# Optimization experiments

Measured on AMD Instinct MI355X. Metric: run time of the kernel, lower is better.

Reference implementation:

```python
import jax, jax.numpy as jnp
import numpy as np

ALPHA = 0.1
N_NODES = 100000
N_FEATS = 1024
HIDDEN = 64
N_CLASSES = 64
N_EDGES = 3200000


def setup_inputs() -> dict:
    key = jax.random.key(0)
    k1, k2, k3, k4 = jax.random.split(key, 4)
    x = jax.random.normal(k1, (N_NODES, N_FEATS), dtype=jnp.float32)
    lin1_w = jax.random.normal(k2, (N_FEATS, HIDDEN), dtype=jnp.float32) * (1.0 / np.sqrt(N_FEATS))
    lin1_b = jnp.zeros((HIDDEN,), dtype=jnp.float32)
    lin2_w = jax.random.normal(k3, (HIDDEN, N_CLASSES), dtype=jnp.float32) * (1.0 / np.sqrt(HIDDEN))
    lin2_b = jnp.zeros((N_CLASSES,), dtype=jnp.float32)
    edge_index = jax.random.randint(k4, (2, N_EDGES), 0, N_NODES, dtype=jnp.int32)
    return {"x": x, "lin1_w": lin1_w, "lin1_b": lin1_b,
            "lin2_w": lin2_w, "lin2_b": lin2_b,
            "edge_index": edge_index, "K": 10}


def _appnp(h, edge_index, n_nodes, K):
    # GCN normalization with self loops: deg^-1/2 (A + I) deg^-1/2
    loops = jnp.arange(n_nodes, dtype=edge_index.dtype)
    row = jnp.concatenate([edge_index[0], loops])  # target nodes
    col = jnp.concatenate([edge_index[1], loops])  # source nodes
    deg = jax.ops.segment_sum(jnp.ones_like(row, dtype=h.dtype), row,
                              num_segments=n_nodes)
    dinv = jnp.where(deg > 0, jax.lax.rsqrt(jnp.maximum(deg, 1e-12)), 0.0)
    norm = dinv[row] * dinv[col]  # [E+N]

    def step(z, _):
        msg = z[col] * norm[:, None]                     # gather + scale
        agg = jax.ops.segment_sum(msg, row, num_segments=n_nodes)
        z = (1.0 - ALPHA) * agg + ALPHA * h              # teleport to h0
        return z, None

    z, _ = jax.lax.scan(step, h, None, length=K)
    return z


def reference(x, lin1_w, lin1_b, lin2_w, lin2_b, edge_index, K):
    # eval mode: dropout disabled
    h = jax.nn.relu(x @ lin1_w + lin1_b)
    h = h @ lin2_w + lin2_b
    z = _appnp(h, edge_index, x.shape[0], K)
    return jax.nn.log_softmax(z, axis=1)
```

## Files before the change

kernel.cpp:

```cpp
#include <hip/hip_runtime.h>
#include <math.h>


constexpr int KSTEPS = 10;

typedef __attribute__((ext_vector_type(8))) short short8;
typedef __attribute__((ext_vector_type(4))) float f32x4;

static __device__ __forceinline__ unsigned short f2bf(float f) {
    unsigned u = __builtin_bit_cast(unsigned, f);
    unsigned r = (u + 0x7FFFu + ((u >> 16) & 1u)) >> 16;
    return (unsigned short)r;
}
static __device__ __forceinline__ float bf2f(unsigned short b) {
    unsigned u = (unsigned)b << 16;
    return __builtin_bit_cast(float, u);
}
static __device__ __forceinline__ void splitbf(float f, short* hi, short* lo) {
    unsigned u = __builtin_bit_cast(unsigned, f);
    *hi = (short)(u >> 16);
    float rem = f - __builtin_bit_cast(float, u & 0xFFFF0000u);
    *lo = (short)f2bf(rem);
}
static __device__ __forceinline__ unsigned char f2fp8(float f) {
    int p = __builtin_amdgcn_cvt_pk_fp8_f32(f, f, 0, false);
    return (unsigned char)(p & 0xFF);
}
static __device__ __forceinline__ float fp82f(unsigned b) {
    return __builtin_amdgcn_cvt_f32_fp8((int)b, 0);
}


__global__ void k_zero(int* __restrict__ p, int n) {
    int i = blockIdx.x * 256 + threadIdx.x;
    if (i < n) p[i] = 0;
}

__global__ void k_hist(const int* __restrict__ ei, int* __restrict__ btot, int E, int NB) {
    __shared__ int hist[512];
    for (int t = threadIdx.x; t < NB; t += 256) hist[t] = 0;
    __syncthreads();
    int base = blockIdx.x * 4096;
#pragma unroll
    for (int k = 0; k < 16; ++k) {
        int e = base + k * 256 + threadIdx.x;
        if (e < E) atomicAdd(&hist[ei[e] >> 8], 1);
    }
    __syncthreads();
    for (int t = threadIdx.x; t < NB; t += 256) {
        int c = hist[t];
        if (c) atomicAdd(&btot[t], c);
    }
}

__global__ void k_scanb(const int* __restrict__ btot, int* __restrict__ bstart,
                        int* __restrict__ bcur, int* __restrict__ row_ptr,
                        int NB, int N, int E) {
    __shared__ int lds[512];
    int t = threadIdx.x;
    int v0 = (t < NB) ? btot[t] : 0;
    int v = v0;
    lds[t] = v;
    __syncthreads();
    for (int o = 1; o < 512; o <<= 1) {
        int a = (t >= o) ? lds[t - o] : 0;
        __syncthreads();
        v += a;
        lds[t] = v;
        __syncthreads();
    }
    if (t < NB) {
        int ex = v - v0;
        bstart[t] = ex;
        bcur[t] = ex;
    }
    if (t == 0) {
        bstart[NB] = E;
        row_ptr[N] = E;
    }
}

__launch_bounds__(256)
__global__ void k_part(const int* __restrict__ ei, int* __restrict__ bcur,
                       unsigned* __restrict__ ebuf, int E, int NB) {
    __shared__ int hist[512], rebase[512], lcur[512];
    for (int t = threadIdx.x; t < NB; t += 256) { hist[t] = 0; lcur[t] = 0; }
    __syncthreads();
    int base = blockIdx.x * 4096;
    int r[16], c[16];
#pragma unroll
    for (int k = 0; k < 16; ++k) {
        int e = base + k * 256 + threadIdx.x;
        bool ok = e < E;
        r[k] = ok ? ei[e] : -1;
        c[k] = ok ? ei[E + e] : 0;
        if (ok) atomicAdd(&hist[r[k] >> 8], 1);
    }
    __syncthreads();
    for (int t = threadIdx.x; t < NB; t += 256) {
        int cnt = hist[t];
        rebase[t] = cnt ? atomicAdd(&bcur[t], cnt) : 0;
    }
    __syncthreads();
#pragma unroll
    for (int k = 0; k < 16; ++k) {
        if (r[k] >= 0) {
            int b = r[k] >> 8;
            int pos = rebase[b] + atomicAdd(&lcur[b], 1);
            ebuf[pos] = (unsigned)c[k] | ((unsigned)(r[k] & 255) << 24);
        }
    }
}

__launch_bounds__(256)
__global__ void k_bucket(const unsigned* __restrict__ ebuf, const int* __restrict__ bstart,
                         int* __restrict__ row_ptr, float* __restrict__ dinv,
                         int* __restrict__ cols, int N) {
    __shared__ int cnt[256], cur[256], lds[256];
    int b = blockIdx.x, t = threadIdx.x;
    int s = bstart[b], e2 = bstart[b + 1];
    cnt[t] = 0;
    __syncthreads();
    for (int i = s + t; i < e2; i += 256) {
        unsigned p = ebuf[i];
        atomicAdd(&cnt[p >> 24], 1);
    }
    __syncthreads();
    int v0 = cnt[t];
    int v = v0;
    lds[t] = v;
    __syncthreads();
    for (int o = 1; o < 256; o <<= 1) {
        int a = (t >= o) ? lds[t - o] : 0;
        __syncthreads();
        v += a;
        lds[t] = v;
        __syncthreads();
    }
    int excl = v - v0;
    int row = (b << 8) + t;
    if (row < N) {
        row_ptr[row] = s + excl;
        dinv[row] = rsqrtf((float)(v0 + 1));
    }
    cur[t] = s + excl;
    __syncthreads();
    for (int i = s + t; i < e2; i += 256) {
        unsigned p = ebuf[i];
        int pos = atomicAdd(&cur[p >> 24], 1);
        cols[pos] = (int)(p & 0x00FFFFFFu);
    }
}

__global__ void k_zrow(unsigned char* __restrict__ a, unsigned char* __restrict__ b,
                       unsigned char* __restrict__ c, int N) {
    int t = threadIdx.x;
    size_t o = (size_t)N * 64 + t;
    a[o] = 0; b[o] = 0; c[o] = 0;
}

__global__ void k_pack_w1(const float* __restrict__ w1, short* __restrict__ w1fh,
                          short* __restrict__ w1fl) {
    int t = blockIdx.x * 256 + threadIdx.x;
    int j = t & 7, lane = (t >> 3) & 63, nb = (t >> 9) & 3, kb = t >> 11;
    int k = kb * 32 + ((lane >> 4) << 3) + j;
    int c = nb * 16 + (lane & 15);
    short hi, lo;
    splitbf(w1[k * 64 + c], &hi, &lo);
    w1fh[t] = hi;
    w1fl[t] = lo;
}

__global__ void k_pack_w2(const float* __restrict__ w2, short* __restrict__ w2fh,
                          short* __restrict__ w2fl) {
    int t = blockIdx.x * 256 + threadIdx.x;
    int j = t & 7, lane = (t >> 3) & 63, nb = (t >> 9) & 3, kb = (t >> 11) & 1;
    int k = kb * 32 + ((lane >> 4) << 3) + j;
    int c = nb * 16 + (lane & 15);
    short hi, lo;
    splitbf(w2[k * 64 + c], &hi, &lo);
    w2fh[t] = hi;
    w2fl[t] = lo;
}

__launch_bounds__(256)
__global__ void k_mlp(const float* __restrict__ x,
                      const short8* __restrict__ w1fh, const short8* __restrict__ w1fl,
                      const float* __restrict__ b1,
                      const short8* __restrict__ w2fh, const short8* __restrict__ w2fl,
                      const float* __restrict__ b2, const float* __restrict__ dinv,
                      unsigned short* __restrict__ ah, unsigned char* __restrict__ u0,
                      int M, int F) {
    __shared__ __align__(16) short c1sh[4][16][64];
    __shared__ __align__(16) short c1sl[4][16][64];
    int tid = threadIdx.x;
    int w = tid >> 6, lane = tid & 63;
    int hi = lane >> 4, lx = lane & 15;
    int rbase = blockIdx.x * 64 + w * 16;
    int row = rbase + lx;
    size_t rowc = (row < M) ? (size_t)row : (size_t)(M - 1);
    const float* xr = x + rowc * (size_t)F + hi * 8;

    f32x4 acc[4];
#pragma unroll
    for (int nb = 0; nb < 4; ++nb) acc[nb] = (f32x4){0.f, 0.f, 0.f, 0.f};

    int KK = F >> 5;
#pragma unroll 2
    for (int kk = 0; kk < KK; ++kk) {
        float4 a0 = *reinterpret_cast<const float4*>(xr + kk * 32);
        float4 a1 = *reinterpret_cast<const float4*>(xr + kk * 32 + 4);
        float av[8] = {a0.x, a0.y, a0.z, a0.w, a1.x, a1.y, a1.z, a1.w};
        short8 afh, afl;
#pragma unroll
        for (int j = 0; j < 8; ++j) {
            short h8, l8;
            splitbf(av[j], &h8, &l8);
            afh[j] = h8;
            afl[j] = l8;
        }
#pragma unroll
        for (int nb = 0; nb < 4; ++nb) {
            short8 bfh = w1fh[(kk * 4 + nb) * 64 + lane];
            short8 bfl = w1fl[(kk * 4 + nb) * 64 + lane];
            acc[nb] = __builtin_amdgcn_mfma_f32_16x16x32_bf16(afh, bfh, acc[nb], 0, 0, 0);
            acc[nb] = __builtin_amdgcn_mfma_f32_16x16x32_bf16(afl, bfh, acc[nb], 0, 0, 0);
            acc[nb] = __builtin_amdgcn_mfma_f32_16x16x32_bf16(afh, bfl, acc[nb], 0, 0, 0);
        }
    }

    short* myh = &c1sh[w][0][0];
    short* myl = &c1sl[w][0][0];
#pragma unroll
    for (int nb = 0; nb < 4; ++nb) {
        int col = nb * 16 + lx;
        float bb = b1[col];
#pragma unroll
        for (int r = 0; r < 4; ++r) {
            int rr = hi * 4 + r;
            float v = fmaxf(acc[nb][r] + bb, 0.f);
            short h8, l8;
            splitbf(v, &h8, &l8);
            myh[rr * 64 + col] = h8;
            myl[rr * 64 + col] = l8;
        }
    }
    __syncthreads();

    f32x4 acc2[4];
#pragma unroll
    for (int nb = 0; nb < 4; ++nb) acc2[nb] = (f32x4){0.f, 0.f, 0.f, 0.f};
#pragma unroll
    for (int kb = 0; kb < 2; ++kb) {
        short8 a2h = *reinterpret_cast<const short8*>(&myh[lx * 64 + kb * 32 + hi * 8]);
        short8 a2l = *reinterpret_cast<const short8*>(&myl[lx * 64 + kb * 32 + hi * 8]);
#pragma unroll
        for (int nb = 0; nb < 4; ++nb) {
            short8 bfh = w2fh[(kb * 4 + nb) * 64 + lane];
            short8 bfl = w2fl[(kb * 4 + nb) * 64 + lane];
            acc2[nb] = __builtin_amdgcn_mfma_f32_16x16x32_bf16(a2h, bfh, acc2[nb], 0, 0, 0);
            acc2[nb] = __builtin_amdgcn_mfma_f32_16x16x32_bf16(a2l, bfh, acc2[nb], 0, 0, 0);
            acc2[nb] = __builtin_amdgcn_mfma_f32_16x16x32_bf16(a2h, bfl, acc2[nb], 0, 0, 0);
        }
    }

#pragma unroll
    for (int r = 0; r < 4; ++r) {
        int orow = rbase + hi * 4 + r;
        float dv = (orow < M) ? dinv[orow] : 0.f;
#pragma unroll
        for (int nb = 0; nb < 4; ++nb) {
            int col = nb * 16 + lx;
            if (orow < M) {
                float v = acc2[nb][r] + b2[col];
                ah[(size_t)orow * 64 + col] = f2bf(0.1f * v);
                u0[(size_t)orow * 64 + col] = f2fp8(dv * v);
            }
        }
    }
}

__global__ void k_prop(const unsigned char* __restrict__ uin, const unsigned short* __restrict__ ah,
                       const float* __restrict__ dinv, const int* __restrict__ row_ptr,
                       const int* __restrict__ cols, unsigned char* __restrict__ uout,
                       int n, int E) {
    int wid = threadIdx.x >> 6;
    int lane = threadIdx.x & 63;
    int half = lane >> 5, fl = lane & 31;
    int r0 = blockIdx.x * 8 + wid * 2;
    int ra = min(r0, n - 1), rb = min(r0 + 1, n - 1);
    int ea = row_ptr[ra], enda = row_ptr[ra + 1];
    int eb = row_ptr[rb], endb = row_ptr[rb + 1];
    int trips = (max(enda - ea, endb - eb) + 7) >> 3;
    int e0 = half ? eb : ea;
    int end_ = half ? endb : enda;
    int r = half ? rb : ra;

    float s0 = 0.f, s1 = 0.f, s2 = 0.f, s3 = 0.f, s4 = 0.f, s5 = 0.f, s6 = 0.f, s7 = 0.f;
    float t0 = 0.f, t1 = 0.f, t2 = 0.f, t3 = 0.f, t4 = 0.f, t5 = 0.f, t6 = 0.f, t7 = 0.f;
    for (int t = 0; t < trips; ++t) {
        int base = e0 + t * 8;
        int ep0 = base,     ep1 = base + 1, ep2 = base + 2, ep3 = base + 3;
        int ep4 = base + 4, ep5 = base + 5, ep6 = base + 6, ep7 = base + 7;
        int c0 = (ep0 < end_) ? cols[min(ep0, E - 1)] : n;
        int c1 = (ep1 < end_) ? cols[min(ep1, E - 1)] : n;
        int c2 = (ep2 < end_) ? cols[min(ep2, E - 1)] : n;
        int c3 = (ep3 < end_) ? cols[min(ep3, E - 1)] : n;
        int c4 = (ep4 < end_) ? cols[min(ep4, E - 1)] : n;
        int c5 = (ep5 < end_) ? cols[min(ep5, E - 1)] : n;
        int c6 = (ep6 < end_) ? cols[min(ep6, E - 1)] : n;
        int c7 = (ep7 < end_) ? cols[min(ep7, E - 1)] : n;
        unsigned v0 = *reinterpret_cast<const unsigned short*>(uin + (size_t)c0 * 64 + fl * 2);
        unsigned v1 = *reinterpret_cast<const unsigned short*>(uin + (size_t)c1 * 64 + fl * 2);
        unsigned v2 = *reinterpret_cast<const unsigned short*>(uin + (size_t)c2 * 64 + fl * 2);
        unsigned v3 = *reinterpret_cast<const unsigned short*>(uin + (size_t)c3 * 64 + fl * 2);
        unsigned v4 = *reinterpret_cast<const unsigned short*>(uin + (size_t)c4 * 64 + fl * 2);
        unsigned v5 = *reinterpret_cast<const unsigned short*>(uin + (size_t)c5 * 64 + fl * 2);
        unsigned v6 = *reinterpret_cast<const unsigned short*>(uin + (size_t)c6 * 64 + fl * 2);
        unsigned v7 = *reinterpret_cast<const unsigned short*>(uin + (size_t)c7 * 64 + fl * 2);
        s0 += fp82f(v0 & 0xFF); t0 += fp82f(v0 >> 8);
        s1 += fp82f(v1 & 0xFF); t1 += fp82f(v1 >> 8);
        s2 += fp82f(v2 & 0xFF); t2 += fp82f(v2 >> 8);
        s3 += fp82f(v3 & 0xFF); t3 += fp82f(v3 >> 8);
        s4 += fp82f(v4 & 0xFF); t4 += fp82f(v4 >> 8);
        s5 += fp82f(v5 & 0xFF); t5 += fp82f(v5 >> 8);
        s6 += fp82f(v6 & 0xFF); t6 += fp82f(v6 >> 8);
        s7 += fp82f(v7 & 0xFF); t7 += fp82f(v7 >> 8);
    }
    float sa = ((s0 + s1) + (s2 + s3)) + ((s4 + s5) + (s6 + s7));
    float sb = ((t0 + t1) + (t2 + t3)) + ((t4 + t5) + (t6 + t7));
    unsigned sv = *reinterpret_cast<const unsigned short*>(uin + (size_t)r * 64 + fl * 2);
    unsigned av = *reinterpret_cast<const unsigned*>(ah + (size_t)r * 64 + fl * 2);
    float di = dinv[r];
    float w = 0.9f * di;
    float z0 = fmaf(w, sa + fp82f(sv & 0xFF), bf2f((unsigned short)(av & 0xFFFF)));
    float z1 = fmaf(w, sb + fp82f(sv >> 8), bf2f((unsigned short)(av >> 16)));
    if (blockIdx.x * 8 + wid * 2 + half < n) {
        unsigned short o = (unsigned short)((unsigned)f2fp8(di * z0) | ((unsigned)f2fp8(di * z1) << 8));
        *reinterpret_cast<unsigned short*>(uout + (size_t)r * 64 + fl * 2) = o;
    }
}

__global__ void k_prop_lsm(const unsigned char* __restrict__ uin, const unsigned short* __restrict__ ah,
                           const float* __restrict__ dinv, const int* __restrict__ row_ptr,
                           const int* __restrict__ cols, float* __restrict__ out,
                           int n, int E) {
    int wid = threadIdx.x >> 6;
    int lane = threadIdx.x & 63;
    int half = lane >> 5, fl = lane & 31;
    int r0 = blockIdx.x * 8 + wid * 2;
    int ra = min(r0, n - 1), rb = min(r0 + 1, n - 1);
    int ea = row_ptr[ra], enda = row_ptr[ra + 1];
    int eb = row_ptr[rb], endb = row_ptr[rb + 1];
    int trips = (max(enda - ea, endb - eb) + 7) >> 3;
    int e0 = half ? eb : ea;
    int end_ = half ? endb : enda;
    int r = half ? rb : ra;

    float s0 = 0.f, s1 = 0.f, s2 = 0.f, s3 = 0.f, s4 = 0.f, s5 = 0.f, s6 = 0.f, s7 = 0.f;
    float t0 = 0.f, t1 = 0.f, t2 = 0.f, t3 = 0.f, t4 = 0.f, t5 = 0.f, t6 = 0.f, t7 = 0.f;
    for (int t = 0; t < trips; ++t) {
        int base = e0 + t * 8;
        int ep0 = base,     ep1 = base + 1, ep2 = base + 2, ep3 = base + 3;
        int ep4 = base + 4, ep5 = base + 5, ep6 = base + 6, ep7 = base + 7;
        int c0 = (ep0 < end_) ? cols[min(ep0, E - 1)] : n;
        int c1 = (ep1 < end_) ? cols[min(ep1, E - 1)] : n;
        int c2 = (ep2 < end_) ? cols[min(ep2, E - 1)] : n;
        int c3 = (ep3 < end_) ? cols[min(ep3, E - 1)] : n;
        int c4 = (ep4 < end_) ? cols[min(ep4, E - 1)] : n;
        int c5 = (ep5 < end_) ? cols[min(ep5, E - 1)] : n;
        int c6 = (ep6 < end_) ? cols[min(ep6, E - 1)] : n;
        int c7 = (ep7 < end_) ? cols[min(ep7, E - 1)] : n;
        unsigned v0 = *reinterpret_cast<const unsigned short*>(uin + (size_t)c0 * 64 + fl * 2);
        unsigned v1 = *reinterpret_cast<const unsigned short*>(uin + (size_t)c1 * 64 + fl * 2);
        unsigned v2 = *reinterpret_cast<const unsigned short*>(uin + (size_t)c2 * 64 + fl * 2);
        unsigned v3 = *reinterpret_cast<const unsigned short*>(uin + (size_t)c3 * 64 + fl * 2);
        unsigned v4 = *reinterpret_cast<const unsigned short*>(uin + (size_t)c4 * 64 + fl * 2);
        unsigned v5 = *reinterpret_cast<const unsigned short*>(uin + (size_t)c5 * 64 + fl * 2);
        unsigned v6 = *reinterpret_cast<const unsigned short*>(uin + (size_t)c6 * 64 + fl * 2);
        unsigned v7 = *reinterpret_cast<const unsigned short*>(uin + (size_t)c7 * 64 + fl * 2);
        s0 += fp82f(v0 & 0xFF); t0 += fp82f(v0 >> 8);
        s1 += fp82f(v1 & 0xFF); t1 += fp82f(v1 >> 8);
        s2 += fp82f(v2 & 0xFF); t2 += fp82f(v2 >> 8);
        s3 += fp82f(v3 & 0xFF); t3 += fp82f(v3 >> 8);
        s4 += fp82f(v4 & 0xFF); t4 += fp82f(v4 >> 8);
        s5 += fp82f(v5 & 0xFF); t5 += fp82f(v5 >> 8);
        s6 += fp82f(v6 & 0xFF); t6 += fp82f(v6 >> 8);
        s7 += fp82f(v7 & 0xFF); t7 += fp82f(v7 >> 8);
    }
    float sa = ((s0 + s1) + (s2 + s3)) + ((s4 + s5) + (s6 + s7));
    float sb = ((t0 + t1) + (t2 + t3)) + ((t4 + t5) + (t6 + t7));
    unsigned sv = *reinterpret_cast<const unsigned short*>(uin + (size_t)r * 64 + fl * 2);
    unsigned av = *reinterpret_cast<const unsigned*>(ah + (size_t)r * 64 + fl * 2);
    float di = dinv[r];
    float w = 0.9f * di;
    float z0 = fmaf(w, sa + fp82f(sv & 0xFF), bf2f((unsigned short)(av & 0xFFFF)));
    float z1 = fmaf(w, sb + fp82f(sv >> 8), bf2f((unsigned short)(av >> 16)));
    float m = fmaxf(z0, z1);
#pragma unroll
    for (int o = 1; o <= 16; o <<= 1) m = fmaxf(m, __shfl_xor(m, o, 64));
    float s = expf(z0 - m) + expf(z1 - m);
#pragma unroll
    for (int o = 1; o <= 16; o <<= 1) s += __shfl_xor(s, o, 64);
    float ls = m + logf(s);
    if (blockIdx.x * 8 + wid * 2 + half < n) {
        float2 o2 = make_float2(z0 - ls, z1 - ls);
        *reinterpret_cast<float2*>(out + (size_t)r * 64 + fl * 2) = o2;
    }
}

extern "C" void kernel_launch(void* const* d_in, const int* in_sizes, int n_in,
                              void* d_out, int out_size, void* d_ws, size_t ws_size,
                              hipStream_t stream) {
    const float* x  = (const float*)d_in[0];
    const float* w1 = (const float*)d_in[1];
    const float* b1 = (const float*)d_in[2];
    const float* w2 = (const float*)d_in[3];
    const float* b2 = (const float*)d_in[4];
    const int*   ei = (const int*)d_in[5];

    int F = in_sizes[1] / 64;
    int N = in_sizes[0] / F;
    int E = in_sizes[5] / 2;
    int NB = (N + 255) >> 8;

    char* p = (char*)d_ws;
    auto alloc = [&](size_t bytes) {
        void* r = (void*)p;
        p += (bytes + 255) & ~(size_t)255;
        return r;
    };
    unsigned short* ah   = (unsigned short*)alloc((size_t)N * 64 * 2);
    unsigned char*  u0   = (unsigned char*)alloc((size_t)(N + 1) * 64);
    unsigned char*  uA   = (unsigned char*)alloc((size_t)(N + 1) * 64);
    unsigned char*  uB   = (unsigned char*)alloc((size_t)(N + 1) * 64);
    float* dinv    = (float*)alloc((size_t)N * 4);
    int*   row_ptr = (int*)alloc((size_t)(N + 1) * 4);
    int*   btot    = (int*)alloc(2048);
    int*   bstart  = (int*)alloc(2048);
    int*   bcur    = (int*)alloc(2048);
    unsigned* ebuf = (unsigned*)alloc((size_t)E * 4);
    int*   cols    = (int*)alloc((size_t)E * 4);
    short* w1fh    = (short*)alloc((size_t)F * 64 * 2);
    short* w1fl    = (short*)alloc((size_t)F * 64 * 2);
    short* w2fh    = (short*)alloc((size_t)64 * 64 * 2);
    short* w2fl    = (short*)alloc((size_t)64 * 64 * 2);

    int neb = (E + 4095) / 4096;

    k_zero<<<2, 256, 0, stream>>>(btot, NB);
    k_hist<<<neb, 256, 0, stream>>>(ei, btot, E, NB);
    k_scanb<<<1, 512, 0, stream>>>(btot, bstart, bcur, row_ptr, NB, N, E);
    k_part<<<neb, 256, 0, stream>>>(ei, bcur, ebuf, E, NB);
    k_bucket<<<NB, 256, 0, stream>>>(ebuf, bstart, row_ptr, dinv, cols, N);
    k_zrow<<<1, 64, 0, stream>>>(u0, uA, uB, N);
    k_pack_w1<<<(F * 64) / 256, 256, 0, stream>>>(w1, w1fh, w1fl);
    k_pack_w2<<<16, 256, 0, stream>>>(w2, w2fh, w2fl);
    k_mlp<<<(N + 63) / 64, 256, 0, stream>>>(x, (const short8*)w1fh, (const short8*)w1fl, b1,
                                             (const short8*)w2fh, (const short8*)w2fl, b2,
                                             dinv, ah, u0, N, F);

    const unsigned char* uin = u0;
    unsigned char* bufs[2] = {uA, uB};
    int npb = (N + 7) / 8;
    for (int k = 0; k < KSTEPS - 1; ++k) {
        unsigned char* uo = bufs[k & 1];
        k_prop<<<npb, 256, 0, stream>>>(uin, ah, dinv, row_ptr, cols, uo, N, E);
        uin = uo;
    }
    k_prop_lsm<<<npb, 256, 0, stream>>>(uin, ah, dinv, row_ptr, cols, (float*)d_out, N, E);
}
```

Measured before the change: 810.4 us.

## Drop split-bf16 emulation in MLP and streamline fp8 propagation kernels

The MLP previously emulated fp32 precision with hi/lo bf16 splits and three MFMAs per tile. It now uses a single bf16 MFMA per tile with one packed weight array and one shared-memory buffer, and the main loop unroll goes from 2 to 4. The propagation kernels load column indices without clamping, relying on a padded cols allocation, and use the byte-select fp8 conversion and packed fp8 store. This cuts MFMA and conversion work in the x-reading GEMM but lowers precision of the dense layers.

```diff
diff --git a/kernel.cpp b/kernel.cpp
--- a/kernel.cpp
+++ b/kernel.cpp
@@ -16,18 +16,15 @@
     unsigned u = (unsigned)b << 16;
     return __builtin_bit_cast(float, u);
 }
-static __device__ __forceinline__ void splitbf(float f, short* hi, short* lo) {
-    unsigned u = __builtin_bit_cast(unsigned, f);
-    *hi = (short)(u >> 16);
-    float rem = f - __builtin_bit_cast(float, u & 0xFFFF0000u);
-    *lo = (short)f2bf(rem);
-}
 static __device__ __forceinline__ unsigned char f2fp8(float f) {
     int p = __builtin_amdgcn_cvt_pk_fp8_f32(f, f, 0, false);
     return (unsigned char)(p & 0xFF);
 }
-static __device__ __forceinline__ float fp82f(unsigned b) {
-    return __builtin_amdgcn_cvt_f32_fp8((int)b, 0);
+static __device__ __forceinline__ float fp8b0(unsigned v) {
+    return __builtin_amdgcn_cvt_f32_fp8((int)v, 0);
+}
+static __device__ __forceinline__ float fp8b1(unsigned v) {
+    return __builtin_amdgcn_cvt_f32_fp8((int)v, 1);
 }
 
 
@@ -159,40 +156,29 @@
     a[o] = 0; b[o] = 0; c[o] = 0;
 }
 
-__global__ void k_pack_w1(const float* __restrict__ w1, short* __restrict__ w1fh,
-                          short* __restrict__ w1fl) {
+__global__ void k_pack_w1(const float* __restrict__ w1, short* __restrict__ w1f) {
     int t = blockIdx.x * 256 + threadIdx.x;
     int j = t & 7, lane = (t >> 3) & 63, nb = (t >> 9) & 3, kb = t >> 11;
     int k = kb * 32 + ((lane >> 4) << 3) + j;
     int c = nb * 16 + (lane & 15);
-    short hi, lo;
-    splitbf(w1[k * 64 + c], &hi, &lo);
-    w1fh[t] = hi;
-    w1fl[t] = lo;
-}
-
-__global__ void k_pack_w2(const float* __restrict__ w2, short* __restrict__ w2fh,
-                          short* __restrict__ w2fl) {
+    w1f[t] = (short)f2bf(w1[k * 64 + c]);
+}
+
+__global__ void k_pack_w2(const float* __restrict__ w2, short* __restrict__ w2f) {
     int t = blockIdx.x * 256 + threadIdx.x;
     int j = t & 7, lane = (t >> 3) & 63, nb = (t >> 9) & 3, kb = (t >> 11) & 1;
     int k = kb * 32 + ((lane >> 4) << 3) + j;
     int c = nb * 16 + (lane & 15);
-    short hi, lo;
-    splitbf(w2[k * 64 + c], &hi, &lo);
-    w2fh[t] = hi;
-    w2fl[t] = lo;
+    w2f[t] = (short)f2bf(w2[k * 64 + c]);
 }
 
 __launch_bounds__(256)
-__global__ void k_mlp(const float* __restrict__ x,
-                      const short8* __restrict__ w1fh, const short8* __restrict__ w1fl,
-                      const float* __restrict__ b1,
-                      const short8* __restrict__ w2fh, const short8* __restrict__ w2fl,
+__global__ void k_mlp(const float* __restrict__ x, const short8* __restrict__ w1f,
+                      const float* __restrict__ b1, const short8* __restrict__ w2f,
                       const float* __restrict__ b2, const float* __restrict__ dinv,
                       unsigned short* __restrict__ ah, unsigned char* __restrict__ u0,
                       int M, int F) {
-    __shared__ __align__(16) short c1sh[4][16][64];
-    __shared__ __align__(16) short c1sl[4][16][64];
+    __shared__ __align__(16) short c1s[4][16][64];
     int tid = threadIdx.x;
     int w = tid >> 6, lane = tid & 63;
     int hi = lane >> 4, lx = lane & 15;
@@ -206,31 +192,23 @@
     for (int nb = 0; nb < 4; ++nb) acc[nb] = (f32x4){0.f, 0.f, 0.f, 0.f};
 
     int KK = F >> 5;
-#pragma unroll 2
+#pragma unroll 4
     for (int kk = 0; kk < KK; ++kk) {
         float4 a0 = *reinterpret_cast<const float4*>(xr + kk * 32);
         float4 a1 = *reinterpret_cast<const float4*>(xr + kk * 32 + 4);
-        float av[8] = {a0.x, a0.y, a0.z, a0.w, a1.x, a1.y, a1.z, a1.w};
-        short8 afh, afl;
-#pragma unroll
-        for (int j = 0; j < 8; ++j) {
-            short h8, l8;
-            splitbf(av[j], &h8, &l8);
-            afh[j] = h8;
-            afl[j] = l8;
+        short8 af;
+        af[0] = (short)f2bf(a0.x); af[1] = (short)f2bf(a0.y);
+        af[2] = (short)f2bf(a0.z); af[3] = (short)f2bf(a0.w);
+        af[4] = (short)f2bf(a1.x); af[5] = (short)f2bf(a1.y);
+        af[6] = (short)f2bf(a1.z); af[7] = (short)f2bf(a1.w);
+#pragma unroll
+        for (int nb = 0; nb < 4; ++nb) {
+            short8 bf = w1f[(kk * 4 + nb) * 64 + lane];
+            acc[nb] = __builtin_amdgcn_mfma_f32_16x16x32_bf16(af, bf, acc[nb], 0, 0, 0);
         }
-#pragma unroll
-        for (int nb = 0; nb < 4; ++nb) {
-            short8 bfh = w1fh[(kk * 4 + nb) * 64 + lane];
-            short8 bfl = w1fl[(kk * 4 + nb) * 64 + lane];
-            acc[nb] = __builtin_amdgcn_mfma_f32_16x16x32_bf16(afh, bfh, acc[nb], 0, 0, 0);
-            acc[nb] = __builtin_amdgcn_mfma_f32_16x16x32_bf16(afl, bfh, acc[nb], 0, 0, 0);
-            acc[nb] = __builtin_amdgcn_mfma_f32_16x16x32_bf16(afh, bfl, acc[nb], 0, 0, 0);
-        }
-    }
-
-    short* myh = &c1sh[w][0][0];
-    short* myl = &c1sl[w][0][0];
+    }
+
+    short* my = &c1s[w][0][0];
 #pragma unroll
     for (int nb = 0; nb < 4; ++nb) {
         int col = nb * 16 + lx;
@@ -238,11 +216,7 @@
 #pragma unroll
         for (int r = 0; r < 4; ++r) {
             int rr = hi * 4 + r;
-            float v = fmaxf(acc[nb][r] + bb, 0.f);
-            short h8, l8;
-            splitbf(v, &h8, &l8);
-            myh[rr * 64 + col] = h8;
-            myl[rr * 64 + col] = l8;
+            my[rr * 64 + col] = (short)f2bf(fmaxf(acc[nb][r] + bb, 0.f));
         }
     }
     __syncthreads();
@@ -252,15 +226,11 @@
     for (int nb = 0; nb < 4; ++nb) acc2[nb] = (f32x4){0.f, 0.f, 0.f, 0.f};
 #pragma unroll
     for (int kb = 0; kb < 2; ++kb) {
-        short8 a2h = *reinterpret_cast<const short8*>(&myh[lx * 64 + kb * 32 + hi * 8]);
-        short8 a2l = *reinterpret_cast<const short8*>(&myl[lx * 64 + kb * 32 + hi * 8]);
+        short8 af2 = *reinterpret_cast<const short8*>(&my[lx * 64 + kb * 32 + hi * 8]);
 #pragma unroll
         for (int nb = 0; nb < 4; ++nb) {
-            short8 bfh = w2fh[(kb * 4 + nb) * 64 + lane];
-            short8 bfl = w2fl[(kb * 4 + nb) * 64 + lane];
-            acc2[nb] = __builtin_amdgcn_mfma_f32_16x16x32_bf16(a2h, bfh, acc2[nb], 0, 0, 0);
-            acc2[nb] = __builtin_amdgcn_mfma_f32_16x16x32_bf16(a2l, bfh, acc2[nb], 0, 0, 0);
-            acc2[nb] = __builtin_amdgcn_mfma_f32_16x16x32_bf16(a2h, bfl, acc2[nb], 0, 0, 0);
+            short8 bf2 = w2f[(kb * 4 + nb) * 64 + lane];
+            acc2[nb] = __builtin_amdgcn_mfma_f32_16x16x32_bf16(af2, bf2, acc2[nb], 0, 0, 0);
         }
     }
 
@@ -282,8 +252,7 @@
 
 __global__ void k_prop(const unsigned char* __restrict__ uin, const unsigned short* __restrict__ ah,
                        const float* __restrict__ dinv, const int* __restrict__ row_ptr,
-                       const int* __restrict__ cols, unsigned char* __restrict__ uout,
-                       int n, int E) {
+                       const int* __restrict__ cols, unsigned char* __restrict__ uout, int n) {
     int wid = threadIdx.x >> 6;
     int lane = threadIdx.x & 63;
     int half = lane >> 5, fl = lane & 31;
@@ -300,16 +269,16 @@
     float t0 = 0.f, t1 = 0.f, t2 = 0.f, t3 = 0.f, t4 = 0.f, t5 = 0.f, t6 = 0.f, t7 = 0.f;
     for (int t = 0; t < trips; ++t) {
         int base = e0 + t * 8;
-        int ep0 = base,     ep1 = base + 1, ep2 = base + 2, ep3 = base + 3;
-        int ep4 = base + 4, ep5 = base + 5, ep6 = base + 6, ep7 = base + 7;
-        int c0 = (ep0 < end_) ? cols[min(ep0, E - 1)] : n;
-        int c1 = (ep1 < end_) ? cols[min(ep1, E - 1)] : n;
-        int c2 = (ep2 < end_) ? cols[min(ep2, E - 1)] : n;
-        int c3 = (ep3 < end_) ? cols[min(ep3, E - 1)] : n;
-        int c4 = (ep4 < end_) ? cols[min(ep4, E - 1)] : n;
-        int c5 = (ep5 < end_) ? cols[min(ep5, E - 1)] : n;
-        int c6 = (ep6 < end_) ? cols[min(ep6, E - 1)] : n;
-        int c7 = (ep7 < end_) ? cols[min(ep7, E - 1)] : n;
+        int q0 = cols[base],     q1 = cols[base + 1], q2 = cols[base + 2], q3 = cols[base + 3];
+        int q4 = cols[base + 4], q5 = cols[base + 5], q6 = cols[base + 6], q7 = cols[base + 7];
+        int c0 = (base     < end_) ? q0 : n;
+        int c1 = (base + 1 < end_) ? q1 : n;
+        int c2 = (base + 2 < end_) ? q2 : n;
+        int c3 = (base + 3 < end_) ? q3 : n;
+        int c4 = (base + 4 < end_) ? q4 : n;
+        int c5 = (base + 5 < end_) ? q5 : n;
+        int c6 = (base + 6 < end_) ? q6 : n;
+        int c7 = (base + 7 < end_) ? q7 : n;
         unsigned v0 = *reinterpret_cast<const unsigned short*>(uin + (size_t)c0 * 64 + fl * 2);
         unsigned v1 = *reinterpret_cast<const unsigned short*>(uin + (size_t)c1 * 64 + fl * 2);
         unsigned v2 = *reinterpret_cast<const unsigned short*>(uin + (size_t)c2 * 64 + fl * 2);
@@ -318,14 +287,14 @@
         unsigned v5 = *reinterpret_cast<const unsigned short*>(uin + (size_t)c5 * 64 + fl * 2);
         unsigned v6 = *reinterpret_cast<const unsigned short*>(uin + (size_t)c6 * 64 + fl * 2);
         unsigned v7 = *reinterpret_cast<const unsigned short*>(uin + (size_t)c7 * 64 + fl * 2);
-        s0 += fp82f(v0 & 0xFF); t0 += fp82f(v0 >> 8);
-        s1 += fp82f(v1 & 0xFF); t1 += fp82f(v1 >> 8);
-        s2 += fp82f(v2 & 0xFF); t2 += fp82f(v2 >> 8);
-        s3 += fp82f(v3 & 0xFF); t3 += fp82f(v3 >> 8);
-        s4 += fp82f(v4 & 0xFF); t4 += fp82f(v4 >> 8);
-        s5 += fp82f(v5 & 0xFF); t5 += fp82f(v5 >> 8);
-        s6 += fp82f(v6 & 0xFF); t6 += fp82f(v6 >> 8);
-        s7 += fp82f(v7 & 0xFF); t7 += fp82f(v7 >> 8);
+        s0 += fp8b0(v0); t0 += fp8b1(v0);
+        s1 += fp8b0(v1); t1 += fp8b1(v1);
+        s2 += fp8b0(v2); t2 += fp8b1(v2);
+        s3 += fp8b0(v3); t3 += fp8b1(v3);
+        s4 += fp8b0(v4); t4 += fp8b1(v4);
+        s5 += fp8b0(v5); t5 += fp8b1(v5);
+        s6 += fp8b0(v6); t6 += fp8b1(v6);
+        s7 += fp8b0(v7); t7 += fp8b1(v7);
     }
     float sa = ((s0 + s1) + (s2 + s3)) + ((s4 + s5) + (s6 + s7));
     float sb = ((t0 + t1) + (t2 + t3)) + ((t4 + t5) + (t6 + t7));
@@ -333,18 +302,18 @@
     unsigned av = *reinterpret_cast<const unsigned*>(ah + (size_t)r * 64 + fl * 2);
     float di = dinv[r];
     float w = 0.9f * di;
-    float z0 = fmaf(w, sa + fp82f(sv & 0xFF), bf2f((unsigned short)(av & 0xFFFF)));
-    float z1 = fmaf(w, sb + fp82f(sv >> 8), bf2f((unsigned short)(av >> 16)));
+    float z0 = fmaf(w, sa + fp8b0(sv), bf2f((unsigned short)(av & 0xFFFF)));
+    float z1 = fmaf(w, sb + fp8b1(sv), bf2f((unsigned short)(av >> 16)));
     if (blockIdx.x * 8 + wid * 2 + half < n) {
-        unsigned short o = (unsigned short)((unsigned)f2fp8(di * z0) | ((unsigned)f2fp8(di * z1) << 8));
-        *reinterpret_cast<unsigned short*>(uout + (size_t)r * 64 + fl * 2) = o;
+        int o = __builtin_amdgcn_cvt_pk_fp8_f32(di * z0, di * z1, 0, false);
+        *reinterpret_cast<unsigned short*>(uout + (size_t)r * 64 + fl * 2) =
+            (unsigned short)(o & 0xFFFF);
     }
 }
 
 __global__ void k_prop_lsm(const unsigned char* __restrict__ uin, const unsigned short* __restrict__ ah,
                            const float* __restrict__ dinv, const int* __restrict__ row_ptr,
-                           const int* __restrict__ cols, float* __restrict__ out,
-                           int n, int E) {
+                           const int* __restrict__ cols, float* __restrict__ out, int n) {
     int wid = threadIdx.x >> 6;
     int lane = threadIdx.x & 63;
     int half = lane >> 5, fl = lane & 31;
@@ -361,16 +330,16 @@
     float t0 = 0.f, t1 = 0.f, t2 = 0.f, t3 = 0.f, t4 = 0.f, t5 = 0.f, t6 = 0.f, t7 = 0.f;
     for (int t = 0; t < trips; ++t) {
         int base = e0 + t * 8;
-        int ep0 = base,     ep1 = base + 1, ep2 = base + 2, ep3 = base + 3;
-        int ep4 = base + 4, ep5 = base + 5, ep6 = base + 6, ep7 = base + 7;
-        int c0 = (ep0 < end_) ? cols[min(ep0, E - 1)] : n;
-        int c1 = (ep1 < end_) ? cols[min(ep1, E - 1)] : n;
-        int c2 = (ep2 < end_) ? cols[min(ep2, E - 1)] : n;
-        int c3 = (ep3 < end_) ? cols[min(ep3, E - 1)] : n;
-        int c4 = (ep4 < end_) ? cols[min(ep4, E - 1)] : n;
-        int c5 = (ep5 < end_) ? cols[min(ep5, E - 1)] : n;
-        int c6 = (ep6 < end_) ? cols[min(ep6, E - 1)] : n;
-        int c7 = (ep7 < end_) ? cols[min(ep7, E - 1)] : n;
+        int q0 = cols[base],     q1 = cols[base + 1], q2 = cols[base + 2], q3 = cols[base + 3];
+        int q4 = cols[base + 4], q5 = cols[base + 5], q6 = cols[base + 6], q7 = cols[base + 7];
+        int c0 = (base     < end_) ? q0 : n;
+        int c1 = (base + 1 < end_) ? q1 : n;
+        int c2 = (base + 2 < end_) ? q2 : n;
+        int c3 = (base + 3 < end_) ? q3 : n;
+        int c4 = (base + 4 < end_) ? q4 : n;
+        int c5 = (base + 5 < end_) ? q5 : n;
+        int c6 = (base + 6 < end_) ? q6 : n;
+        int c7 = (base + 7 < end_) ? q7 : n;
         unsigned v0 = *reinterpret_cast<const unsigned short*>(uin + (size_t)c0 * 64 + fl * 2);
         unsigned v1 = *reinterpret_cast<const unsigned short*>(uin + (size_t)c1 * 64 + fl * 2);
         unsigned v2 = *reinterpret_cast<const unsigned short*>(uin + (size_t)c2 * 64 + fl * 2);
@@ -379,14 +348,14 @@
         unsigned v5 = *reinterpret_cast<const unsigned short*>(uin + (size_t)c5 * 64 + fl * 2);
         unsigned v6 = *reinterpret_cast<const unsigned short*>(uin + (size_t)c6 * 64 + fl * 2);
         unsigned v7 = *reinterpret_cast<const unsigned short*>(uin + (size_t)c7 * 64 + fl * 2);
-        s0 += fp82f(v0 & 0xFF); t0 += fp82f(v0 >> 8);
-        s1 += fp82f(v1 & 0xFF); t1 += fp82f(v1 >> 8);
-        s2 += fp82f(v2 & 0xFF); t2 += fp82f(v2 >> 8);
-        s3 += fp82f(v3 & 0xFF); t3 += fp82f(v3 >> 8);
-        s4 += fp82f(v4 & 0xFF); t4 += fp82f(v4 >> 8);
-        s5 += fp82f(v5 & 0xFF); t5 += fp82f(v5 >> 8);
-        s6 += fp82f(v6 & 0xFF); t6 += fp82f(v6 >> 8);
-        s7 += fp82f(v7 & 0xFF); t7 += fp82f(v7 >> 8);
+        s0 += fp8b0(v0); t0 += fp8b1(v0);
+        s1 += fp8b0(v1); t1 += fp8b1(v1);
+        s2 += fp8b0(v2); t2 += fp8b1(v2);
+        s3 += fp8b0(v3); t3 += fp8b1(v3);
+        s4 += fp8b0(v4); t4 += fp8b1(v4);
+        s5 += fp8b0(v5); t5 += fp8b1(v5);
+        s6 += fp8b0(v6); t6 += fp8b1(v6);
+        s7 += fp8b0(v7); t7 += fp8b1(v7);
     }
     float sa = ((s0 + s1) + (s2 + s3)) + ((s4 + s5) + (s6 + s7));
     float sb = ((t0 + t1) + (t2 + t3)) + ((t4 + t5) + (t6 + t7));
@@ -394,8 +363,8 @@
     unsigned av = *reinterpret_cast<const unsigned*>(ah + (size_t)r * 64 + fl * 2);
     float di = dinv[r];
     float w = 0.9f * di;
-    float z0 = fmaf(w, sa + fp82f(sv & 0xFF), bf2f((unsigned short)(av & 0xFFFF)));
-    float z1 = fmaf(w, sb + fp82f(sv >> 8), bf2f((unsigned short)(av >> 16)));
+    float z0 = fmaf(w, sa + fp8b0(sv), bf2f((unsigned short)(av & 0xFFFF)));
+    float z1 = fmaf(w, sb + fp8b1(sv), bf2f((unsigned short)(av >> 16)));
     float m = fmaxf(z0, z1);
 #pragma unroll
     for (int o = 1; o <= 16; o <<= 1) m = fmaxf(m, __shfl_xor(m, o, 64));
@@ -440,11 +409,9 @@
     int*   bstart  = (int*)alloc(2048);
     int*   bcur    = (int*)alloc(2048);
     unsigned* ebuf = (unsigned*)alloc((size_t)E * 4);
-    int*   cols    = (int*)alloc((size_t)E * 4);
-    short* w1fh    = (short*)alloc((size_t)F * 64 * 2);
-    short* w1fl    = (short*)alloc((size_t)F * 64 * 2);
-    short* w2fh    = (short*)alloc((size_t)64 * 64 * 2);
-    short* w2fl    = (short*)alloc((size_t)64 * 64 * 2);
+    int*   cols    = (int*)alloc((size_t)(E + 256) * 4);
+    short* w1f     = (short*)alloc((size_t)F * 64 * 2);
+    short* w2f     = (short*)alloc((size_t)64 * 64 * 2);
 
     int neb = (E + 4095) / 4096;
 
@@ -454,10 +421,10 @@
     k_part<<<neb, 256, 0, stream>>>(ei, bcur, ebuf, E, NB);
     k_bucket<<<NB, 256, 0, stream>>>(ebuf, bstart, row_ptr, dinv, cols, N);
     k_zrow<<<1, 64, 0, stream>>>(u0, uA, uB, N);
-    k_pack_w1<<<(F * 64) / 256, 256, 0, stream>>>(w1, w1fh, w1fl);
-    k_pack_w2<<<16, 256, 0, stream>>>(w2, w2fh, w2fl);
-    k_mlp<<<(N + 63) / 64, 256, 0, stream>>>(x, (const short8*)w1fh, (const short8*)w1fl, b1,
-                                             (const short8*)w2fh, (const short8*)w2fl, b2,
+    k_pack_w1<<<(F * 64) / 256, 256, 0, stream>>>(w1, w1f);
+    k_pack_w2<<<16, 256, 0, stream>>>(w2, w2f);
+    k_mlp<<<(N + 63) / 64, 256, 0, stream>>>(x, (const short8*)w1f, b1,
+                                             (const short8*)w2f, b2,
                                              dinv, ah, u0, N, F);
 
     const unsigned char* uin = u0;
@@ -465,8 +432,8 @@
     int npb = (N + 7) / 8;
     for (int k = 0; k < KSTEPS - 1; ++k) {
         unsigned char* uo = bufs[k & 1];
-        k_prop<<<npb, 256, 0, stream>>>(uin, ah, dinv, row_ptr, cols, uo, N, E);
+        k_prop<<<npb, 256, 0, stream>>>(uin, ah, dinv, row_ptr, cols, uo, N);
         uin = uo;
     }
-    k_prop_lsm<<<npb, 256, 0, stream>>>(uin, ah, dinv, row_ptr, cols, (float*)d_out, N, E);
-}
+    k_prop_lsm<<<npb, 256, 0, stream>>>(uin, ah, dinv, row_ptr, cols, (float*)d_out, N);
+}
```

Result: faster. 678.6 us (-16.3%).
